# Performance work log

Measured on AMD Instinct MI355X. Metric: run time of the kernel, lower is better.

Reference implementation:

```python
import jax, jax.numpy as jnp
import numpy as np

B, S = 32, 2048
ENC2 = 1024   # encoder_hidden*2
DEC = 1024    # decoder_hidden
ATT = 1024    # attention_hidden


def setup_inputs() -> dict:
    key = jax.random.key(0)
    ks = jax.random.split(key, 8)
    s_enc = 1.0 / np.sqrt(ENC2)
    s_dec = 1.0 / np.sqrt(DEC)
    s_e = 1.0 / np.sqrt(ATT)
    return {
        "decoder_hidden": jax.random.normal(ks[0], (B, DEC), jnp.float32),
        "encoder_outputs": jax.random.normal(ks[1], (B, S, ENC2), jnp.float32),
        "mask": jnp.ones((B, S), dtype=bool),
        "W_enc": jax.random.uniform(ks[2], (ENC2, ATT), jnp.float32, -s_enc, s_enc),
        "b_enc": jax.random.uniform(ks[3], (ATT,), jnp.float32, -s_enc, s_enc),
        "W_dec": jax.random.uniform(ks[4], (DEC, ATT), jnp.float32, -s_dec, s_dec),
        "b_dec": jax.random.uniform(ks[5], (ATT,), jnp.float32, -s_dec, s_dec),
        "w_e": jax.random.uniform(ks[6], (ATT,), jnp.float32, -s_e, s_e),
        "b_e": jax.random.uniform(ks[7], (), jnp.float32, -s_e, s_e),
    }


def reference(decoder_hidden, encoder_outputs, mask, W_enc, b_enc, W_dec, b_dec, w_e, b_e):
    # encoder_proj: (B, S, ATT)
    encoder_proj = jnp.einsum('bse,ea->bsa', encoder_outputs, W_enc) + b_enc
    # decoder_proj: (B, 1, ATT)
    decoder_proj = (decoder_hidden @ W_dec + b_dec)[:, None, :]
    # energy: (B, S) -- Linear(ATT,1) then squeeze
    energy = jnp.einsum('bsa,a->bs', jnp.tanh(encoder_proj + decoder_proj), w_e) + b_e
    energy = jnp.where(mask, energy, -jnp.inf)
    attention_weights = jax.nn.softmax(energy, axis=1)           # (B, S)
    context = jnp.einsum('bs,bse->be', attention_weights, encoder_outputs)  # (B, ENC2)
    return context, attention_weights
```

## Files before the change

### kernel.cpp

```cpp
#include <hip/hip_runtime.h>
#include <math.h>

#define S_LEN 2048
#define ENC2  1024
#define DEC_H 1024
#define ATT   1024
#define BATCH 32

typedef __attribute__((ext_vector_type(8)))  short short8;
typedef __attribute__((ext_vector_type(4)))  short s4;
typedef __attribute__((ext_vector_type(16))) float f32x16;

#define DP_OFF (ATT * ENC2 * 2)

__device__ __forceinline__ unsigned short f2bf(float f) {
    unsigned int u = __float_as_uint(f);
    return (unsigned short)((u + 0x7FFFu + ((u >> 16) & 1u)) >> 16);
}

__device__ __forceinline__ float tanh_fast(float x) {
    float ax = fabsf(x);
    float e = __expf(-2.0f * ax);
    float t = (1.0f - e) / (1.0f + e);
    return copysignf(t, x);
}

__global__ void k_pack(const float* __restrict__ W, unsigned short* __restrict__ P) {
    int t  = threadIdx.x;
    int kb = blockIdx.x;
    int nb = blockIdx.y * 4 + (t >> 6);
    int l  = t & 63;
    int n  = nb * 32 + (l & 31);
    int k0 = kb * 16 + ((l >> 5) * 8);
    short8 v;
#pragma unroll
    for (int j = 0; j < 8; ++j)
        v[j] = (short)f2bf(W[(size_t)(k0 + j) * ATT + n]);
    *(short8*)(P + (((size_t)kb * 32 + nb) * 64 + l) * 8) = v;
}

__global__ void k_dproj(const float* __restrict__ dec, const float* __restrict__ Wd,
                        const float* __restrict__ b_dec, const float* __restrict__ b_enc,
                        float* __restrict__ dp) {
    int n = blockIdx.x * 256 + threadIdx.x;
    int b = blockIdx.y;
    const float* dh = dec + b * DEC_H;
    float a0 = 0, a1 = 0, a2 = 0, a3 = 0;
#pragma unroll 8
    for (int k = 0; k < DEC_H; k += 4) {
        a0 = fmaf(dh[k + 0], Wd[(size_t)(k + 0) * ATT + n], a0);
        a1 = fmaf(dh[k + 1], Wd[(size_t)(k + 1) * ATT + n], a1);
        a2 = fmaf(dh[k + 2], Wd[(size_t)(k + 2) * ATT + n], a2);
        a3 = fmaf(dh[k + 3], Wd[(size_t)(k + 3) * ATT + n], a3);
    }
    dp[b * ATT + n] = b_dec[n] + b_enc[n] + ((a0 + a1) + (a2 + a3));
}

__launch_bounds__(256, 4)
__global__ void k_energy(const float* __restrict__ enc,
                         const short* __restrict__ BP,
                         const float* __restrict__ dp,
                         const float* __restrict__ w_e,
                         float* __restrict__ ew)
{
    __shared__ short As[2][64][64];
    __shared__ float e_lds[64];

    const int tid   = threadIdx.x;
    const int bid   = blockIdx.x;
    const int swz   = (bid & 7) * 512 + (bid >> 3);
    const int stripe = swz >> 2;
    const int nq    = swz & 3;
    const int r0    = stripe << 6;
    const int b     = stripe >> 5;

    const int lane = tid & 63;
    const int wid  = tid >> 6;
    const int col  = lane & 31;
    const int hi   = lane >> 5;
    const int hi16 = hi << 4;
    const int xr   = (col & 7) << 4;

    float dv[2], wv[2];
#pragma unroll
    for (int nf = 0; nf < 2; ++nf) {
        int n = nq * 256 + wid * 64 + nf * 32 + col;
        dv[nf] = dp[b * ATT + n];
        wv[nf] = w_e[n];
    }

    const char* bpp = (const char*)BP + (size_t)(nq * 8 + wid * 2) * 1024 + lane * 16;

    f32x16 acc[2][2];
#pragma unroll
    for (int mf = 0; mf < 2; ++mf)
#pragma unroll
        for (int nf = 0; nf < 2; ++nf)
#pragma unroll
            for (int r = 0; r < 16; ++r) acc[mf][nf][r] = 0.0f;

    short8 bb0[2], bb1[2];
    bb0[0] = *(const short8*)(bpp);
    bb0[1] = *(const short8*)(bpp + 1024);
    bb1[0] = *(const short8*)(bpp + 32768);
    bb1[1] = *(const short8*)(bpp + 32768 + 1024);

#pragma unroll
    for (int i = 0; i < 4; ++i) {
        int u = i * 256 + tid, row = u >> 4, fs = u & 15;
        float4 fv = *(const float4*)(enc + ((size_t)(r0 + row) << 10) + (fs << 2));
        s4 v; v[0] = (short)f2bf(fv.x); v[1] = (short)f2bf(fv.y);
              v[2] = (short)f2bf(fv.z); v[3] = (short)f2bf(fv.w);
        *(s4*)((char*)As + row * 128 + ((fs * 8) ^ ((row & 7) << 4))) = v;
    }
    __syncthreads();

#pragma unroll 1
    for (int ph = 0; ph < 16; ++ph) {
        float4 f[4];
        const bool have = (ph < 15);
        if (have) {
#pragma unroll
            for (int i = 0; i < 4; ++i) {
                int u = i * 256 + tid, row = u >> 4, fs = u & 15;
                f[i] = *(const float4*)(enc + ((size_t)(r0 + row) << 10)
                                            + ((ph + 1) << 6) + (fs << 2));
            }
        }

        const char* ab    = (const char*)As + ((ph & 1) << 13);
        const char* arow0 = ab + col * 128;
        const char* arow1 = ab + (col + 32) * 128;
        const int kbase = ph << 2;
#pragma unroll
        for (int t = 0; t < 4; t += 2) {
            {
                int off = ((t << 5) + hi16) ^ xr;
                short8 a0 = *(const short8*)(arow0 + off);
                short8 a1 = *(const short8*)(arow1 + off);
                acc[0][0] = __builtin_amdgcn_mfma_f32_32x32x16_bf16(a0, bb0[0], acc[0][0], 0, 0, 0);
                acc[0][1] = __builtin_amdgcn_mfma_f32_32x32x16_bf16(a0, bb0[1], acc[0][1], 0, 0, 0);
                acc[1][0] = __builtin_amdgcn_mfma_f32_32x32x16_bf16(a1, bb0[0], acc[1][0], 0, 0, 0);
                acc[1][1] = __builtin_amdgcn_mfma_f32_32x32x16_bf16(a1, bb0[1], acc[1][1], 0, 0, 0);
                size_t ro = (size_t)((kbase + t + 2) & 63) << 15;
                bb0[0] = *(const short8*)(bpp + ro);
                bb0[1] = *(const short8*)(bpp + ro + 1024);
            }
            {
                int off = (((t + 1) << 5) + hi16) ^ xr;
                short8 a0 = *(const short8*)(arow0 + off);
                short8 a1 = *(const short8*)(arow1 + off);
                acc[0][0] = __builtin_amdgcn_mfma_f32_32x32x16_bf16(a0, bb1[0], acc[0][0], 0, 0, 0);
                acc[0][1] = __builtin_amdgcn_mfma_f32_32x32x16_bf16(a0, bb1[1], acc[0][1], 0, 0, 0);
                acc[1][0] = __builtin_amdgcn_mfma_f32_32x32x16_bf16(a1, bb1[0], acc[1][0], 0, 0, 0);
                acc[1][1] = __builtin_amdgcn_mfma_f32_32x32x16_bf16(a1, bb1[1], acc[1][1], 0, 0, 0);
                size_t ro = (size_t)((kbase + t + 3) & 63) << 15;
                bb1[0] = *(const short8*)(bpp + ro);
                bb1[1] = *(const short8*)(bpp + ro + 1024);
            }
        }

        __syncthreads();
        if (have) {
            char* dst = (char*)As + (((ph + 1) & 1) << 13);
#pragma unroll
            for (int i = 0; i < 4; ++i) {
                int u = i * 256 + tid, row = u >> 4, fs = u & 15;
                float4 fv = f[i];
                s4 v; v[0] = (short)f2bf(fv.x); v[1] = (short)f2bf(fv.y);
                      v[2] = (short)f2bf(fv.z); v[3] = (short)f2bf(fv.w);
                *(s4*)(dst + row * 128 + ((fs * 8) ^ ((row & 7) << 4))) = v;
            }
        }
        __syncthreads();
    }

    float ep[32];
#pragma unroll
    for (int mf = 0; mf < 2; ++mf)
#pragma unroll
        for (int reg = 0; reg < 16; ++reg) {
            float s = fmaf(wv[0], tanh_fast(acc[mf][0][reg] + dv[0]),
                           wv[1] * tanh_fast(acc[mf][1][reg] + dv[1]));
            ep[mf * 16 + reg] = s;
        }
#pragma unroll
    for (int d = 1; d < 32; d <<= 1)
#pragma unroll
        for (int j = 0; j < 32; ++j)
            ep[j] += __shfl_xor(ep[j], d, 64);

    if (tid < 64) e_lds[tid] = 0.0f;
    __syncthreads();
    if (col == 0) {
#pragma unroll
        for (int j = 0; j < 32; ++j) {
            int reg = j & 15;
            int row = (j >> 4) * 32 + (reg & 3) + 8 * (reg >> 2) + 4 * hi;
            atomicAdd(&e_lds[row], ep[j]);
        }
    }
    __syncthreads();
    if (tid < 64) atomicAdd(&ew[r0 + tid], e_lds[tid]);
}

__global__ void k_softmax(const int* __restrict__ mask, const float* __restrict__ b_e,
                          float* __restrict__ out) {
    int b = blockIdx.x, tid = threadIdx.x;
    float* ew = out + BATCH * ATT + (size_t)b * S_LEN;
    const int* mk = mask + (size_t)b * S_LEN;
    float be = b_e[0];
    float v[8];
#pragma unroll
    for (int i = 0; i < 8; ++i) {
        int s = i * 256 + tid;
        float e = ew[s] + be;
        v[i] = mk[s] ? e : -INFINITY;
    }
    float m = v[0];
#pragma unroll
    for (int i = 1; i < 8; ++i) m = fmaxf(m, v[i]);
#pragma unroll
    for (int d = 1; d < 64; d <<= 1) m = fmaxf(m, __shfl_xor(m, d, 64));
    __shared__ float red[4], red2[4];
    int w = tid >> 6;
    if ((tid & 63) == 0) red[w] = m;
    __syncthreads();
    m = fmaxf(fmaxf(red[0], red[1]), fmaxf(red[2], red[3]));
    float s = 0.0f;
#pragma unroll
    for (int i = 0; i < 8; ++i) { v[i] = __expf(v[i] - m); s += v[i]; }
#pragma unroll
    for (int d = 1; d < 64; d <<= 1) s += __shfl_xor(s, d, 64);
    if ((tid & 63) == 0) red2[w] = s;
    __syncthreads();
    s = red2[0] + red2[1] + red2[2] + red2[3];
    float inv = 1.0f / s;
#pragma unroll
    for (int i = 0; i < 8; ++i) ew[i * 256 + tid] = v[i] * inv;
    float* ctx = out + (size_t)b * ATT;
#pragma unroll
    for (int i = 0; i < 4; ++i) ctx[i * 256 + tid] = 0.0f;
}

__global__ void k_context(const float* __restrict__ enc, const float* __restrict__ wgt,
                          float* __restrict__ ctx) {
    int sx = blockIdx.x, b = blockIdx.y, tid = threadIdx.x;
    __shared__ float wsh[64];
    if (tid < 64) wsh[tid] = wgt[(size_t)b * S_LEN + sx * 64 + tid];
    __syncthreads();
    const float* ep = enc + ((size_t)b * S_LEN + sx * 64) * ENC2 + tid * 4;
    float ax = 0, ay = 0, az = 0, aw = 0;
    for (int s0 = 0; s0 < 64; s0 += 8) {
        float4 r[8];
#pragma unroll
        for (int j = 0; j < 8; ++j)
            r[j] = *(const float4*)(ep + (size_t)(s0 + j) * ENC2);
#pragma unroll
        for (int j = 0; j < 8; ++j) {
            float w = wsh[s0 + j];
            ax = fmaf(w, r[j].x, ax); ay = fmaf(w, r[j].y, ay);
            az = fmaf(w, r[j].z, az); aw = fmaf(w, r[j].w, aw);
        }
    }
    float* c = ctx + (size_t)b * ATT + tid * 4;
    atomicAdd(c + 0, ax); atomicAdd(c + 1, ay);
    atomicAdd(c + 2, az); atomicAdd(c + 3, aw);
}

extern "C" void kernel_launch(void* const* d_in, const int* in_sizes, int n_in,
                              void* d_out, int out_size, void* d_ws, size_t ws_size,
                              hipStream_t stream) {
    (void)in_sizes; (void)n_in; (void)out_size; (void)ws_size;
    const float* dec   = (const float*)d_in[0];
    const float* enc   = (const float*)d_in[1];
    const int*   mask  = (const int*)d_in[2];
    const float* W_enc = (const float*)d_in[3];
    const float* b_enc = (const float*)d_in[4];
    const float* W_dec = (const float*)d_in[5];
    const float* b_dec = (const float*)d_in[6];
    const float* w_e   = (const float*)d_in[7];
    const float* b_e   = (const float*)d_in[8];

    float* out = (float*)d_out;
    unsigned short* BP = (unsigned short*)d_ws;
    float* dp = (float*)((char*)d_ws + DP_OFF);
    float* ew = out + BATCH * ATT;

    hipMemsetAsync(ew, 0, (size_t)BATCH * S_LEN * sizeof(float), stream);
    k_pack<<<dim3(64, 8), 256, 0, stream>>>(W_enc, BP);
    k_dproj<<<dim3(4, 32), 256, 0, stream>>>(dec, W_dec, b_dec, b_enc, dp);
    k_energy<<<4096, 256, 0, stream>>>(enc, (const short*)BP, dp, w_e, ew);
    k_softmax<<<32, 256, 0, stream>>>(mask, b_e, out);
    k_context<<<dim3(32, 32), 256, 0, stream>>>(enc, ew, out);
}
```

Before: 574.1 us.

## Pre-convert encoder outputs to swizzled bf16 and load via global_load_lds

Adds a pre-pass that converts the fp32 encoder outputs once into a pre-swizzled bf16 tile layout in workspace. The energy GEMM then streams A tiles straight into LDS with global_load_lds and 128-wide K phases, replacing the per-block fp32 load and convert that was repeated for each of the four N-quarter blocks. The context reduction also switches from float atomics to partial sums plus a separate reduce kernel. Both paths depend on workspace size and fall back to the old kernels when it is too small. The cost is an extra 128MB bf16 write and read plus two more launches.

```diff
diff --git a/kernel.cpp b/kernel.cpp
--- a/kernel.cpp
+++ b/kernel.cpp
@@ -11,7 +11,11 @@
 typedef __attribute__((ext_vector_type(4)))  short s4;
 typedef __attribute__((ext_vector_type(16))) float f32x16;
 
-#define DP_OFF (ATT * ENC2 * 2)
+#define DP_OFF  (2u << 20)
+#define CTX_OFF (4u << 20)
+#define AP_OFF  (8u << 20)
+#define NEED_CTX  ((size_t)(8u << 20))
+#define NEED_FULL ((size_t)(8u << 20) + 134217728ull)
 
 __device__ __forceinline__ unsigned short f2bf(float f) {
     unsigned int u = __float_as_uint(f);
@@ -23,6 +27,12 @@
     float e = __expf(-2.0f * ax);
     float t = (1.0f - e) / (1.0f + e);
     return copysignf(t, x);
+}
+
+__device__ __forceinline__ void gload16(const void* g, void* l) {
+    __builtin_amdgcn_global_load_lds(
+        (const __attribute__((address_space(1))) void*)g,
+        (__attribute__((address_space(3))) void*)l, 16, 0, 0);
 }
 
 __global__ void k_pack(const float* __restrict__ W, unsigned short* __restrict__ P) {
@@ -37,6 +47,30 @@
     for (int j = 0; j < 8; ++j)
         v[j] = (short)f2bf(W[(size_t)(k0 + j) * ATT + n]);
     *(short8*)(P + (((size_t)kb * 32 + nb) * 64 + l) * 8) = v;
+}
+
+__global__ void k_cvtA(const float* __restrict__ enc, char* __restrict__ AP) {
+    const int tid = threadIdx.x;
+#pragma unroll 1
+    for (int it = 0; it < 16; ++it) {
+        int g = blockIdx.x * 4096 + it * 256 + tid;
+        int stripe = g >> 13;
+        int rem    = g & 8191;
+        int ph     = rem >> 10;
+        int u      = rem & 1023;
+        int row    = u >> 4;
+        int slot   = u & 15;
+        const float* src = enc + (((size_t)stripe * 64 + row) << 10) + (ph << 7) + (slot << 3);
+        float4 f0 = *(const float4*)src;
+        float4 f1 = *(const float4*)(src + 4);
+        short8 v;
+        v[0] = (short)f2bf(f0.x); v[1] = (short)f2bf(f0.y);
+        v[2] = (short)f2bf(f0.z); v[3] = (short)f2bf(f0.w);
+        v[4] = (short)f2bf(f1.x); v[5] = (short)f2bf(f1.y);
+        v[6] = (short)f2bf(f1.z); v[7] = (short)f2bf(f1.w);
+        *(short8*)(AP + ((size_t)stripe << 17) + (ph << 14) + row * 256
+                      + ((slot << 4) ^ ((row & 15) << 4))) = v;
+    }
 }
 
 __global__ void k_dproj(const float* __restrict__ dec, const float* __restrict__ Wd,
@@ -57,29 +91,29 @@
 }
 
 __launch_bounds__(256, 4)
-__global__ void k_energy(const float* __restrict__ enc,
-                         const short* __restrict__ BP,
-                         const float* __restrict__ dp,
-                         const float* __restrict__ w_e,
-                         float* __restrict__ ew)
+__global__ void k_energy_f(const char* __restrict__ AP,
+                           const short* __restrict__ BP,
+                           const float* __restrict__ dp,
+                           const float* __restrict__ w_e,
+                           float* __restrict__ ew)
 {
-    __shared__ short As[2][64][64];
-    __shared__ float e_lds[64];
-
-    const int tid   = threadIdx.x;
-    const int bid   = blockIdx.x;
-    const int swz   = (bid & 7) * 512 + (bid >> 3);
+    __shared__ short As[2][64][128];
+    float* e_lds = (float*)As;
+
+    const int tid    = threadIdx.x;
+    const int bid    = blockIdx.x;
+    const int swz    = (bid & 7) * 512 + (bid >> 3);
     const int stripe = swz >> 2;
-    const int nq    = swz & 3;
-    const int r0    = stripe << 6;
-    const int b     = stripe >> 5;
+    const int nq     = swz & 3;
+    const int r0     = stripe << 6;
+    const int b      = stripe >> 5;
 
     const int lane = tid & 63;
     const int wid  = tid >> 6;
     const int col  = lane & 31;
     const int hi   = lane >> 5;
     const int hi16 = hi << 4;
-    const int xr   = (col & 7) << 4;
+    const int xr   = (col & 15) << 4;
 
     float dv[2], wv[2];
 #pragma unroll
@@ -89,7 +123,8 @@
         wv[nf] = w_e[n];
     }
 
-    const char* bpp = (const char*)BP + (size_t)(nq * 8 + wid * 2) * 1024 + lane * 16;
+    const char* bpp    = (const char*)BP + (size_t)(nq * 8 + wid * 2) * 1024 + lane * 16;
+    const char* apbase = AP + ((size_t)stripe << 17);
 
     f32x16 acc[2][2];
 #pragma unroll
@@ -105,6 +140,115 @@
     bb1[0] = *(const short8*)(bpp + 32768);
     bb1[1] = *(const short8*)(bpp + 32768 + 1024);
 
+#pragma unroll
+    for (int i = 0; i < 4; ++i)
+        gload16(apbase + (wid * 4 + i) * 1024 + lane * 16,
+                (short*)As + (wid * 4 + i) * 512);
+    __syncthreads();
+
+#pragma unroll 1
+    for (int ph = 0; ph < 8; ++ph) {
+        if (ph < 7) {
+            const char* s = apbase + ((ph + 1) << 14);
+            short* d = (short*)As + (((ph + 1) & 1) << 13);
+#pragma unroll
+            for (int i = 0; i < 4; ++i)
+                gload16(s + (wid * 4 + i) * 1024 + lane * 16, d + (wid * 4 + i) * 512);
+        }
+        const char* ab    = (const char*)As + ((ph & 1) << 14);
+        const char* arow0 = ab + col * 256;
+        const char* arow1 = ab + (col + 32) * 256;
+#pragma unroll
+        for (int t = 0; t < 8; t += 2) {
+            const int kb = (ph << 3) + t;
+            {
+                int off = ((t << 5) + hi16) ^ xr;
+                short8 a0 = *(const short8*)(arow0 + off);
+                short8 a1 = *(const short8*)(arow1 + off);
+                acc[0][0] = __builtin_amdgcn_mfma_f32_32x32x16_bf16(a0, bb0[0], acc[0][0], 0, 0, 0);
+                acc[0][1] = __builtin_amdgcn_mfma_f32_32x32x16_bf16(a0, bb0[1], acc[0][1], 0, 0, 0);
+                acc[1][0] = __builtin_amdgcn_mfma_f32_32x32x16_bf16(a1, bb0[0], acc[1][0], 0, 0, 0);
+                acc[1][1] = __builtin_amdgcn_mfma_f32_32x32x16_bf16(a1, bb0[1], acc[1][1], 0, 0, 0);
+                size_t ro = (size_t)((kb + 2) & 63) << 15;
+                bb0[0] = *(const short8*)(bpp + ro);
+                bb0[1] = *(const short8*)(bpp + ro + 1024);
+            }
+            {
+                int off = (((t + 1) << 5) + hi16) ^ xr;
+                short8 a0 = *(const short8*)(arow0 + off);
+                short8 a1 = *(const short8*)(arow1 + off);
+                acc[0][0] = __builtin_amdgcn_mfma_f32_32x32x16_bf16(a0, bb1[0], acc[0][0], 0, 0, 0);
+                acc[0][1] = __builtin_amdgcn_mfma_f32_32x32x16_bf16(a0, bb1[1], acc[0][1], 0, 0, 0);
+                acc[1][0] = __builtin_amdgcn_mfma_f32_32x32x16_bf16(a1, bb1[0], acc[1][0], 0, 0, 0);
+                acc[1][1] = __builtin_amdgcn_mfma_f32_32x32x16_bf16(a1, bb1[1], acc[1][1], 0, 0, 0);
+                size_t ro = (size_t)((kb + 3) & 63) << 15;
+                bb1[0] = *(const short8*)(bpp + ro);
+                bb1[1] = *(const short8*)(bpp + ro + 1024);
+            }
+        }
+        __syncthreads();
+    }
+
+    float ep[32];
+#pragma unroll
+    for (int mf = 0; mf < 2; ++mf)
+#pragma unroll
+        for (int reg = 0; reg < 16; ++reg)
+            ep[mf * 16 + reg] = fmaf(wv[0], tanh_fast(acc[mf][0][reg] + dv[0]),
+                                     wv[1] * tanh_fast(acc[mf][1][reg] + dv[1]));
+#pragma unroll
+    for (int d = 1; d < 32; d <<= 1)
+#pragma unroll
+        for (int j = 0; j < 32; ++j)
+            ep[j] += __shfl_xor(ep[j], d, 64);
+
+    if (tid < 64) e_lds[tid] = 0.0f;
+    __syncthreads();
+    if (col == 0) {
+#pragma unroll
+        for (int j = 0; j < 32; ++j) {
+            int reg = j & 15;
+            int row = (j >> 4) * 32 + (reg & 3) + 8 * (reg >> 2) + 4 * hi;
+            atomicAdd(&e_lds[row], ep[j]);
+        }
+    }
+    __syncthreads();
+    if (tid < 64) atomicAdd(&ew[r0 + tid], e_lds[tid]);
+}
+
+__launch_bounds__(256, 4)
+__global__ void k_energy_v6(const float* __restrict__ enc, const short* __restrict__ BP,
+                            const float* __restrict__ dp, const float* __restrict__ w_e,
+                            float* __restrict__ ew)
+{
+    __shared__ short As[2][64][64];
+    __shared__ float e_lds[64];
+    const int tid = threadIdx.x;
+    const int bid = blockIdx.x;
+    const int swz = (bid & 7) * 512 + (bid >> 3);
+    const int stripe = swz >> 2;
+    const int nq = swz & 3;
+    const int r0 = stripe << 6;
+    const int b  = stripe >> 5;
+    const int lane = tid & 63, wid = tid >> 6, col = lane & 31, hi = lane >> 5;
+    const int hi16 = hi << 4, xr = (col & 7) << 4;
+    float dv[2], wv[2];
+#pragma unroll
+    for (int nf = 0; nf < 2; ++nf) {
+        int n = nq * 256 + wid * 64 + nf * 32 + col;
+        dv[nf] = dp[b * ATT + n]; wv[nf] = w_e[n];
+    }
+    const char* bpp = (const char*)BP + (size_t)(nq * 8 + wid * 2) * 1024 + lane * 16;
+    f32x16 acc[2][2];
+#pragma unroll
+    for (int mf = 0; mf < 2; ++mf)
+#pragma unroll
+        for (int nf = 0; nf < 2; ++nf)
+#pragma unroll
+            for (int r = 0; r < 16; ++r) acc[mf][nf][r] = 0.0f;
+    short8 bb0[2], bb1[2];
+    bb0[0] = *(const short8*)(bpp);         bb0[1] = *(const short8*)(bpp + 1024);
+    bb1[0] = *(const short8*)(bpp + 32768); bb1[1] = *(const short8*)(bpp + 32768 + 1024);
 #pragma unroll
     for (int i = 0; i < 4; ++i) {
         int u = i * 256 + tid, row = u >> 4, fs = u & 15;
@@ -114,7 +258,6 @@
         *(s4*)((char*)As + row * 128 + ((fs * 8) ^ ((row & 7) << 4))) = v;
     }
     __syncthreads();
-
 #pragma unroll 1
     for (int ph = 0; ph < 16; ++ph) {
         float4 f[4];
@@ -123,11 +266,9 @@
 #pragma unroll
             for (int i = 0; i < 4; ++i) {
                 int u = i * 256 + tid, row = u >> 4, fs = u & 15;
-                f[i] = *(const float4*)(enc + ((size_t)(r0 + row) << 10)
-                                            + ((ph + 1) << 6) + (fs << 2));
-            }
-        }
-
+                f[i] = *(const float4*)(enc + ((size_t)(r0 + row) << 10) + ((ph + 1) << 6) + (fs << 2));
+            }
+        }
         const char* ab    = (const char*)As + ((ph & 1) << 13);
         const char* arow0 = ab + col * 128;
         const char* arow1 = ab + (col + 32) * 128;
@@ -143,8 +284,7 @@
                 acc[1][0] = __builtin_amdgcn_mfma_f32_32x32x16_bf16(a1, bb0[0], acc[1][0], 0, 0, 0);
                 acc[1][1] = __builtin_amdgcn_mfma_f32_32x32x16_bf16(a1, bb0[1], acc[1][1], 0, 0, 0);
                 size_t ro = (size_t)((kbase + t + 2) & 63) << 15;
-                bb0[0] = *(const short8*)(bpp + ro);
-                bb0[1] = *(const short8*)(bpp + ro + 1024);
+                bb0[0] = *(const short8*)(bpp + ro); bb0[1] = *(const short8*)(bpp + ro + 1024);
             }
             {
                 int off = (((t + 1) << 5) + hi16) ^ xr;
@@ -155,11 +295,9 @@
                 acc[1][0] = __builtin_amdgcn_mfma_f32_32x32x16_bf16(a1, bb1[0], acc[1][0], 0, 0, 0);
                 acc[1][1] = __builtin_amdgcn_mfma_f32_32x32x16_bf16(a1, bb1[1], acc[1][1], 0, 0, 0);
                 size_t ro = (size_t)((kbase + t + 3) & 63) << 15;
-                bb1[0] = *(const short8*)(bpp + ro);
-                bb1[1] = *(const short8*)(bpp + ro + 1024);
-            }
-        }
-
+                bb1[0] = *(const short8*)(bpp + ro); bb1[1] = *(const short8*)(bpp + ro + 1024);
+            }
+        }
         __syncthreads();
         if (have) {
             char* dst = (char*)As + (((ph + 1) & 1) << 13);
@@ -174,22 +312,18 @@
         }
         __syncthreads();
     }
-
     float ep[32];
 #pragma unroll
     for (int mf = 0; mf < 2; ++mf)
 #pragma unroll
-        for (int reg = 0; reg < 16; ++reg) {
-            float s = fmaf(wv[0], tanh_fast(acc[mf][0][reg] + dv[0]),
-                           wv[1] * tanh_fast(acc[mf][1][reg] + dv[1]));
-            ep[mf * 16 + reg] = s;
-        }
+        for (int reg = 0; reg < 16; ++reg)
+            ep[mf * 16 + reg] = fmaf(wv[0], tanh_fast(acc[mf][0][reg] + dv[0]),
+                                     wv[1] * tanh_fast(acc[mf][1][reg] + dv[1]));
 #pragma unroll
     for (int d = 1; d < 32; d <<= 1)
 #pragma unroll
         for (int j = 0; j < 32; ++j)
             ep[j] += __shfl_xor(ep[j], d, 64);
-
     if (tid < 64) e_lds[tid] = 0.0f;
     __syncthreads();
     if (col == 0) {
@@ -243,8 +377,8 @@
     for (int i = 0; i < 4; ++i) ctx[i * 256 + tid] = 0.0f;
 }
 
-__global__ void k_context(const float* __restrict__ enc, const float* __restrict__ wgt,
-                          float* __restrict__ ctx) {
+__global__ void k_context_p(const float* __restrict__ enc, const float* __restrict__ wgt,
+                            float* __restrict__ ctxp) {
     int sx = blockIdx.x, b = blockIdx.y, tid = threadIdx.x;
     __shared__ float wsh[64];
     if (tid < 64) wsh[tid] = wgt[(size_t)b * S_LEN + sx * 64 + tid];
@@ -263,6 +397,40 @@
             az = fmaf(w, r[j].z, az); aw = fmaf(w, r[j].w, aw);
         }
     }
+    float4 o; o.x = ax; o.y = ay; o.z = az; o.w = aw;
+    *(float4*)(ctxp + ((size_t)b * 32 + sx) * ATT + tid * 4) = o;
+}
+
+__global__ void k_ctx_red(const float* __restrict__ ctxp, float* __restrict__ out) {
+    int n = blockIdx.x * 256 + threadIdx.x;
+    int b = blockIdx.y;
+    float s = 0.0f;
+#pragma unroll
+    for (int sx = 0; sx < 32; ++sx)
+        s += ctxp[((size_t)b * 32 + sx) * ATT + n];
+    out[(size_t)b * ATT + n] = s;
+}
+
+__global__ void k_context_a(const float* __restrict__ enc, const float* __restrict__ wgt,
+                            float* __restrict__ ctx) {
+    int sx = blockIdx.x, b = blockIdx.y, tid = threadIdx.x;
+    __shared__ float wsh[64];
+    if (tid < 64) wsh[tid] = wgt[(size_t)b * S_LEN + sx * 64 + tid];
+    __syncthreads();
+    const float* ep = enc + ((size_t)b * S_LEN + sx * 64) * ENC2 + tid * 4;
+    float ax = 0, ay = 0, az = 0, aw = 0;
+    for (int s0 = 0; s0 < 64; s0 += 8) {
+        float4 r[8];
+#pragma unroll
+        for (int j = 0; j < 8; ++j)
+            r[j] = *(const float4*)(ep + (size_t)(s0 + j) * ENC2);
+#pragma unroll
+        for (int j = 0; j < 8; ++j) {
+            float w = wsh[s0 + j];
+            ax = fmaf(w, r[j].x, ax); ay = fmaf(w, r[j].y, ay);
+            az = fmaf(w, r[j].z, az); aw = fmaf(w, r[j].w, aw);
+        }
+    }
     float* c = ctx + (size_t)b * ATT + tid * 4;
     atomicAdd(c + 0, ax); atomicAdd(c + 1, ay);
     atomicAdd(c + 2, az); atomicAdd(c + 3, aw);
@@ -271,7 +439,7 @@
 extern "C" void kernel_launch(void* const* d_in, const int* in_sizes, int n_in,
                               void* d_out, int out_size, void* d_ws, size_t ws_size,
                               hipStream_t stream) {
-    (void)in_sizes; (void)n_in; (void)out_size; (void)ws_size;
+    (void)in_sizes; (void)n_in; (void)out_size;
     const float* dec   = (const float*)d_in[0];
     const float* enc   = (const float*)d_in[1];
     const int*   mask  = (const int*)d_in[2];
@@ -284,13 +452,28 @@
 
     float* out = (float*)d_out;
     unsigned short* BP = (unsigned short*)d_ws;
-    float* dp = (float*)((char*)d_ws + DP_OFF);
-    float* ew = out + BATCH * ATT;
+    float* dp   = (float*)((char*)d_ws + DP_OFF);
+    float* ctxp = (float*)((char*)d_ws + CTX_OFF);
+    char*  AP   = (char*)d_ws + AP_OFF;
+    float* ew   = out + BATCH * ATT;
+
+    const bool fastA = ws_size >= NEED_FULL;
+    const bool pctx  = ws_size >= NEED_CTX;
 
     hipMemsetAsync(ew, 0, (size_t)BATCH * S_LEN * sizeof(float), stream);
     k_pack<<<dim3(64, 8), 256, 0, stream>>>(W_enc, BP);
     k_dproj<<<dim3(4, 32), 256, 0, stream>>>(dec, W_dec, b_dec, b_enc, dp);
-    k_energy<<<4096, 256, 0, stream>>>(enc, (const short*)BP, dp, w_e, ew);
+    if (fastA) {
+        k_cvtA<<<2048, 256, 0, stream>>>(enc, AP);
+        k_energy_f<<<4096, 256, 0, stream>>>(AP, (const short*)BP, dp, w_e, ew);
+    } else {
+        k_energy_v6<<<4096, 256, 0, stream>>>(enc, (const short*)BP, dp, w_e, ew);
+    }
     k_softmax<<<32, 256, 0, stream>>>(mask, b_e, out);
-    k_context<<<dim3(32, 32), 256, 0, stream>>>(enc, ew, out);
-}
+    if (pctx) {
+        k_context_p<<<dim3(32, 32), 256, 0, stream>>>(enc, ew, ctxp);
+        k_ctx_red<<<dim3(4, 32), 256, 0, stream>>>(ctxp, out);
+    } else {
+        k_context_a<<<dim3(32, 32), 256, 0, stream>>>(enc, ew, out);
+    }
+}
```

New measurement: 648.5 us. 12.9% more time.
